# Kernel optimization log

Measured on AMD Instinct MI355X. Metric: run time of the kernel, lower is better.

## Reference

```python
import jax, jax.numpy as jnp
import numpy as np

EPS = 1e-8  # torch F.cosine_similarity default eps
NEG = -1e9  # masked_fill value


def setup_inputs() -> dict:
    key = jax.random.key(0)
    k1, k2, k3 = jax.random.split(key, 3)
    B, Sq, Sk, D = 4, 2048, 2048, 1024
    query = jax.random.normal(k1, (B, Sq, 1, D), dtype=jnp.float32)
    key_t = jax.random.normal(k2, (B, 1, Sk, D), dtype=jnp.float32)
    mask = jax.random.randint(k3, (B, Sk), 0, 2, dtype=jnp.int32)
    return {"query": query, "key": key_t, "mask": mask}


def reference(query, key, mask):
    # query: [B, Sq, 1, D], key: [B, 1, Sk, D]
    q = query[:, :, 0, :]  # [B, Sq, D]
    k = key[:, 0, :, :]    # [B, Sk, D]
    # cosine_similarity(q, k, dim=3) = (q.k) / (max(|q|,eps) * max(|k|,eps))
    qn = jnp.maximum(jnp.linalg.norm(q, axis=-1), EPS)  # [B, Sq]
    kn = jnp.maximum(jnp.linalg.norm(k, axis=-1), EPS)  # [B, Sk]
    dot = jnp.einsum('bqd,bkd->bqk', q, k)              # [B, Sq, Sk]
    scores = dot / (qn[:, :, None] * kn[:, None, :])
    # mask.unsqueeze(1).repeat(1, Sq, 1) -> broadcast [B, 1, Sk] over Sq
    scores = jnp.where(mask[:, None, :] == 0, NEG, scores)
    return scores
```

## Files before the change

### kernel.cpp

```cpp
#include <hip/hip_runtime.h>
#include <hip/hip_bf16.h>
#include <stdint.h>


constexpr int B_  = 4;
constexpr int SQ  = 2048;
constexpr int SK  = 2048;
constexpr int D_  = 1024;
constexpr int BM  = 128;
constexpr int BN  = 128;
constexpr int BK  = 64;

typedef __attribute__((ext_vector_type(8)))  short    short8;
typedef __attribute__((ext_vector_type(4)))  float    f32x4;
typedef __attribute__((ext_vector_type(16))) float    f32x16;
typedef __attribute__((ext_vector_type(4)))  unsigned uint4v;
typedef unsigned int u32;

__device__ inline unsigned pack_bf16(float lo, float hi) {
  union { float f; unsigned u; } a, b;
  a.f = lo; b.f = hi;
  return __builtin_amdgcn_perm(b.u, a.u, 0x07060302u);
}

__device__ inline void async_ld16(const void* g, void* l) {
  __builtin_amdgcn_global_load_lds((const __attribute__((address_space(1))) u32*)g,
                                   (__attribute__((address_space(3))) u32*)l, 16, 0, 0);
}

constexpr int ROWS_Q = B_ * SQ;
constexpr int ROWS_T = B_ * (SQ + SK);

__global__ __launch_bounds__(256) void convert_norm(
    const float* __restrict__ Q, const float* __restrict__ Km,
    unsigned short* __restrict__ Qb, unsigned short* __restrict__ Kb,
    float* __restrict__ invQ, float* __restrict__ invK)
{
  const int row  = blockIdx.x * 4 + (threadIdx.x >> 6);
  const int lane = threadIdx.x & 63;

  const float* src; unsigned short* dst; float* inv;
  if (row < ROWS_Q) {
    src = Q  + (size_t)row * D_;
    dst = Qb + (size_t)row * D_;
    inv = invQ + row;
  } else {
    int r = row - ROWS_Q;
    src = Km + (size_t)r * D_;
    dst = Kb + (size_t)r * D_;
    inv = invK + r;
  }

  const f32x4* s4 = (const f32x4*)(src + lane * 16);
  f32x4 v[4];
  #pragma unroll
  for (int i = 0; i < 4; ++i) v[i] = s4[i];

  float ss = 0.0f;
  unsigned p[8];
  #pragma unroll
  for (int i = 0; i < 4; ++i) {
    p[2*i]   = pack_bf16(v[i].x, v[i].y);
    p[2*i+1] = pack_bf16(v[i].z, v[i].w);
    ss += v[i].x*v[i].x + v[i].y*v[i].y + v[i].z*v[i].z + v[i].w*v[i].w;
  }
  uint4v w0 = {p[0], p[1], p[2], p[3]};
  uint4v w1 = {p[4], p[5], p[6], p[7]};
  uint4v* d4 = (uint4v*)(dst + lane * 16);
  d4[0] = w0; d4[1] = w1;

  #pragma unroll
  for (int off = 32; off > 0; off >>= 1) ss += __shfl_xor(ss, off);
  if (lane == 0) *inv = 1.0f / fmaxf(sqrtf(ss), 1e-8f);
}

__global__ __launch_bounds__(256, 4) void ca_gemm_bf(
    const unsigned short* __restrict__ Qb,
    const unsigned short* __restrict__ Kb,
    const float* __restrict__ invQ,
    const float* __restrict__ invK,
    const int*   __restrict__ mask,
    float*       __restrict__ out)
{
  __shared__ __align__(16) unsigned short As[BM * BK];
  __shared__ __align__(16) unsigned short Bs[BN * BK];

  const int tid  = threadIdx.x;
  const int lane = tid & 63;
  const int w    = tid >> 6;
  const int b    = blockIdx.z;
  const int tm0  = blockIdx.y * BM;
  const int tn0  = blockIdx.x * BN;

  const int srow   = lane >> 3;
  const int gchunk = (lane & 7) ^ srow;

  const char* qrow = (const char*)(Qb + ((size_t)b * SQ + tm0 + w * 32 + srow) * D_) + gchunk * 16;
  const char* krow = (const char*)(Kb + ((size_t)b * SK + tn0 + w * 32 + srow) * D_) + gchunk * 16;
  const size_t rstep8 = (size_t)8 * D_ * 2;

  unsigned short* ldsA = &As[(size_t)(w * 32) * BK];
  unsigned short* ldsB = &Bs[(size_t)(w * 32) * BK];

  f32x16 acc[2][2];
  #pragma unroll
  for (int i = 0; i < 2; ++i)
    #pragma unroll
    for (int j = 0; j < 2; ++j)
      #pragma unroll
      for (int r = 0; r < 16; ++r) acc[i][j][r] = 0.0f;

  const int wm = (w >> 1) * 64;
  const int wn = (w & 1) * 64;
  const int ln = lane & 31;
  const int h  = lane >> 5;

  for (int k0 = 0; k0 < D_; k0 += BK) {
    __syncthreads();
    const size_t kb = (size_t)k0 * 2;
    #pragma unroll
    for (int i = 0; i < 4; ++i)
      async_ld16(qrow + kb + i * rstep8, ldsA + i * 8 * BK);
    #pragma unroll
    for (int i = 0; i < 4; ++i)
      async_ld16(krow + kb + i * rstep8, ldsB + i * 8 * BK);
    __syncthreads();

    #pragma unroll
    for (int s = 0; s < 4; ++s) {
      const int c = 2 * s + h;
      const int ra0 = wm + ln, ra1 = wm + 32 + ln;
      const int rb0 = wn + ln, rb1 = wn + 32 + ln;
      short8 a0 = *(const short8*)&As[(size_t)ra0 * BK + (size_t)((c ^ (ra0 & 7)) * 8)];
      short8 a1 = *(const short8*)&As[(size_t)ra1 * BK + (size_t)((c ^ (ra1 & 7)) * 8)];
      short8 b0 = *(const short8*)&Bs[(size_t)rb0 * BK + (size_t)((c ^ (rb0 & 7)) * 8)];
      short8 b1 = *(const short8*)&Bs[(size_t)rb1 * BK + (size_t)((c ^ (rb1 & 7)) * 8)];
      acc[0][0] = __builtin_amdgcn_mfma_f32_32x32x16_bf16(a0, b0, acc[0][0], 0, 0, 0);
      acc[0][1] = __builtin_amdgcn_mfma_f32_32x32x16_bf16(a0, b1, acc[0][1], 0, 0, 0);
      acc[1][0] = __builtin_amdgcn_mfma_f32_32x32x16_bf16(a1, b0, acc[1][0], 0, 0, 0);
      acc[1][1] = __builtin_amdgcn_mfma_f32_32x32x16_bf16(a1, b1, acc[1][1], 0, 0, 0);
    }
  }

  #pragma unroll
  for (int tj = 0; tj < 2; ++tj) {
    const int gc = tn0 + wn + tj * 32 + ln;
    const int mk = mask[b * SK + gc];
    const float ibv = invK[b * SK + gc];
    #pragma unroll
    for (int ti = 0; ti < 2; ++ti) {
      #pragma unroll
      for (int reg = 0; reg < 16; ++reg) {
        const int row = wm + ti * 32 + (reg & 3) + 8 * (reg >> 2) + 4 * h;
        const float iav = invQ[b * SQ + tm0 + row];
        float v = mk ? acc[ti][tj][reg] * iav * ibv : -1000000000.0f;
        out[((size_t)b * SQ + tm0 + row) * SK + gc] = v;
      }
    }
  }
}

constexpr int LDK = 40;

__global__ __launch_bounds__(256, 2) void ca_gemm(
    const float* __restrict__ Q, const float* __restrict__ Km,
    const int* __restrict__ mask, float* __restrict__ out)
{
  __shared__ __align__(16) short As[BM * LDK];
  __shared__ __align__(16) short Bs[BN * LDK];
  __shared__ float ssA_part[256];
  __shared__ float ssB_part[256];
  __shared__ float invA[BM];
  __shared__ float invB[BN];

  const int tid  = threadIdx.x;
  const int lane = tid & 63;
  const int w    = tid >> 6;
  const int b    = blockIdx.z;
  const int tm0  = blockIdx.y * BM;
  const int tn0  = blockIdx.x * BN;

  const int ra = tid >> 1;
  const int ka = (tid & 1) * 16;

  const float* qp = Q  + ((size_t)b * SQ + tm0 + ra) * D_ + ka;
  const float* kp = Km + ((size_t)b * SK + tn0 + ra) * D_ + ka;

  f32x4 zero4 = {0.0f, 0.0f, 0.0f, 0.0f};
  f32x4 acc[4][4];
  #pragma unroll
  for (int i = 0; i < 4; ++i)
    #pragma unroll
    for (int j = 0; j < 4; ++j) acc[i][j] = zero4;

  float ssA = 0.0f, ssB = 0.0f;

  const int wm = (w >> 1) * 64;
  const int wn = (w & 1) * 64;
  const int lr = lane & 15;
  const int lq = lane >> 4;

  short* aw = &As[ra * LDK + ka];
  short* bw = &Bs[ra * LDK + ka];

  for (int k0 = 0; k0 < D_; k0 += 32) {
    f32x4 av[4], bv[4];
    #pragma unroll
    for (int i = 0; i < 4; ++i) av[i] = *(const f32x4*)(qp + 4 * i);
    #pragma unroll
    for (int i = 0; i < 4; ++i) bv[i] = *(const f32x4*)(kp + 4 * i);
    qp += 32; kp += 32;

    unsigned pa[8], pb[8];
    #pragma unroll
    for (int i = 0; i < 4; ++i) {
      pa[2*i]   = pack_bf16(av[i].x, av[i].y);
      pa[2*i+1] = pack_bf16(av[i].z, av[i].w);
      pb[2*i]   = pack_bf16(bv[i].x, bv[i].y);
      pb[2*i+1] = pack_bf16(bv[i].z, bv[i].w);
      ssA += av[i].x*av[i].x + av[i].y*av[i].y + av[i].z*av[i].z + av[i].w*av[i].w;
      ssB += bv[i].x*bv[i].x + bv[i].y*bv[i].y + bv[i].z*bv[i].z + bv[i].w*bv[i].w;
    }

    __syncthreads();
    {
      uint4v wa0 = {pa[0], pa[1], pa[2], pa[3]};
      uint4v wa1 = {pa[4], pa[5], pa[6], pa[7]};
      uint4v wb0 = {pb[0], pb[1], pb[2], pb[3]};
      uint4v wb1 = {pb[4], pb[5], pb[6], pb[7]};
      *(uint4v*)(aw)     = wa0;
      *(uint4v*)(aw + 8) = wa1;
      *(uint4v*)(bw)     = wb0;
      *(uint4v*)(bw + 8) = wb1;
    }
    __syncthreads();

    short8 af[4], bf[4];
    #pragma unroll
    for (int t = 0; t < 4; ++t)
      af[t] = *(const short8*)&As[(wm + t * 16 + lr) * LDK + lq * 8];
    #pragma unroll
    for (int t = 0; t < 4; ++t)
      bf[t] = *(const short8*)&Bs[(wn + t * 16 + lr) * LDK + lq * 8];

    #pragma unroll
    for (int i = 0; i < 4; ++i)
      #pragma unroll
      for (int j = 0; j < 4; ++j)
        acc[i][j] = __builtin_amdgcn_mfma_f32_16x16x32_bf16(af[i], bf[j], acc[i][j], 0, 0, 0);
  }

  ssA_part[tid] = ssA;
  ssB_part[tid] = ssB;
  __syncthreads();
  if (tid < BM) {
    float s = ssA_part[2 * tid] + ssA_part[2 * tid + 1];
    invA[tid] = 1.0f / fmaxf(sqrtf(s), 1e-8f);
  } else {
    int r = tid - BM;
    float s = ssB_part[2 * r] + ssB_part[2 * r + 1];
    invB[r] = 1.0f / fmaxf(sqrtf(s), 1e-8f);
  }
  __syncthreads();

  #pragma unroll
  for (int tn = 0; tn < 4; ++tn) {
    const int lc = wn + tn * 16 + lr;
    const int gc = tn0 + lc;
    const int mk = mask[b * SK + gc];
    const float ibv = invB[lc];
    #pragma unroll
    for (int tm = 0; tm < 4; ++tm) {
      const int lrow = wm + tm * 16 + lq * 4;
      #pragma unroll
      for (int r = 0; r < 4; ++r) {
        float v = mk ? acc[tm][tn][r] * invA[lrow + r] * ibv : -1000000000.0f;
        out[((size_t)b * SQ + tm0 + lrow + r) * SK + gc] = v;
      }
    }
  }
}

extern "C" void kernel_launch(void* const* d_in, const int* in_sizes, int n_in,
                              void* d_out, int out_size, void* d_ws, size_t ws_size,
                              hipStream_t stream) {
  const float* Q    = (const float*)d_in[0];
  const float* Km   = (const float*)d_in[1];
  const int*   mask = (const int*)d_in[2];
  float*       out  = (float*)d_out;

  const size_t nQ   = (size_t)B_ * SQ * D_;
  const size_t nK   = (size_t)B_ * SK * D_;
  const size_t need = (nQ + nK) * 2 + (size_t)B_ * (SQ + SK) * 4;
  if (ws_size >= need) {
    unsigned short* Qb = (unsigned short*)d_ws;
    unsigned short* Kb = Qb + nQ;
    float*          iQ = (float*)(Kb + nK);
    float*          iK = iQ + (size_t)B_ * SQ;
    convert_norm<<<ROWS_T / 4, 256, 0, stream>>>(Q, Km, Qb, Kb, iQ, iK);
    dim3 grid(SK / BN, SQ / BM, B_);
    ca_gemm_bf<<<grid, dim3(256), 0, stream>>>(Qb, Kb, iQ, iK, mask, out);
  } else {
    dim3 grid(SK / BN, SQ / BM, B_);
    ca_gemm<<<grid, dim3(256), 0, stream>>>(Q, Km, mask, out);
  }
}
```

Measured before the change: 159.3 us.

## Enlarge GEMM tile to 256x256 with triple-buffered async LDS pipeline

The bf16 GEMM kernel moves from 128x128 tiles with BK=64 and 256 threads to 256x256 tiles with BK=32 and 512 threads (8 waves, each computing 128x64). K-slices are staged into three rotating LDS buffers with async global-to-LDS loads and vmcnt-based waits, so loads for future slices overlap MFMA work. Only one barrier per iteration remains instead of two syncthreads. This raises per-block data reuse and hides memory latency, at the cost of a smaller grid (256 blocks), more accumulator registers and a different swizzle.

```diff
diff --git a/kernel.cpp b/kernel.cpp
--- a/kernel.cpp
+++ b/kernel.cpp
@@ -7,9 +7,16 @@
 constexpr int SQ  = 2048;
 constexpr int SK  = 2048;
 constexpr int D_  = 1024;
+
 constexpr int BM  = 128;
 constexpr int BN  = 128;
-constexpr int BK  = 64;
+
+constexpr int BM2 = 256;
+constexpr int BN2 = 256;
+constexpr int BK2 = 32;
+constexpr int NT2 = D_ / BK2;
+constexpr int BUFSH     = BM2 * BK2;
+constexpr int BUFSTRIDE = 2 * BUFSH;
 
 typedef __attribute__((ext_vector_type(8)))  short    short8;
 typedef __attribute__((ext_vector_type(4)))  float    f32x4;
@@ -74,7 +81,7 @@
   if (lane == 0) *inv = 1.0f / fmaxf(sqrtf(ss), 1e-8f);
 }
 
-__global__ __launch_bounds__(256, 4) void ca_gemm_bf(
+__global__ __launch_bounds__(512, 2) void ca_gemm_bf(
     const unsigned short* __restrict__ Qb,
     const unsigned short* __restrict__ Kb,
     const float* __restrict__ invQ,
@@ -82,78 +89,100 @@
     const int*   __restrict__ mask,
     float*       __restrict__ out)
 {
-  __shared__ __align__(16) unsigned short As[BM * BK];
-  __shared__ __align__(16) unsigned short Bs[BN * BK];
+  __shared__ __align__(16) unsigned short lds[3 * BUFSTRIDE];
 
   const int tid  = threadIdx.x;
   const int lane = tid & 63;
   const int w    = tid >> 6;
+  const int wr   = w >> 2;
+  const int wc   = w & 3;
   const int b    = blockIdx.z;
-  const int tm0  = blockIdx.y * BM;
-  const int tn0  = blockIdx.x * BN;
-
-  const int srow   = lane >> 3;
-  const int gchunk = (lane & 7) ^ srow;
-
-  const char* qrow = (const char*)(Qb + ((size_t)b * SQ + tm0 + w * 32 + srow) * D_) + gchunk * 16;
-  const char* krow = (const char*)(Kb + ((size_t)b * SK + tn0 + w * 32 + srow) * D_) + gchunk * 16;
-  const size_t rstep8 = (size_t)8 * D_ * 2;
-
-  unsigned short* ldsA = &As[(size_t)(w * 32) * BK];
-  unsigned short* ldsB = &Bs[(size_t)(w * 32) * BK];
-
-  f32x16 acc[2][2];
-  #pragma unroll
-  for (int i = 0; i < 2; ++i)
-    #pragma unroll
-    for (int j = 0; j < 2; ++j)
+  const int tm0  = blockIdx.y * BM2;
+  const int tn0  = blockIdx.x * BN2;
+
+  const int g = (lane & 3) ^ ((lane >> 3) & 3);
+  const char* qsrc = (const char*)(Qb + ((size_t)b * SQ + tm0 + w * 32 + (lane >> 2)) * D_) + g * 16;
+  const char* ksrc = (const char*)(Kb + ((size_t)b * SK + tn0 + w * 32 + (lane >> 2)) * D_) + g * 16;
+  const size_t RSTEP16 = (size_t)16 * D_ * 2;
+
+  f32x16 acc[4][2];
+  #pragma unroll
+  for (int m = 0; m < 4; ++m)
+    #pragma unroll
+    for (int n = 0; n < 2; ++n)
       #pragma unroll
-      for (int r = 0; r < 16; ++r) acc[i][j][r] = 0.0f;
-
-  const int wm = (w >> 1) * 64;
-  const int wn = (w & 1) * 64;
+      for (int r = 0; r < 16; ++r) acc[m][n][r] = 0.0f;
+
   const int ln = lane & 31;
   const int h  = lane >> 5;
-
-  for (int k0 = 0; k0 < D_; k0 += BK) {
-    __syncthreads();
-    const size_t kb = (size_t)k0 * 2;
-    #pragma unroll
-    for (int i = 0; i < 4; ++i)
-      async_ld16(qrow + kb + i * rstep8, ldsA + i * 8 * BK);
-    #pragma unroll
-    for (int i = 0; i < 4; ++i)
-      async_ld16(krow + kb + i * rstep8, ldsB + i * 8 * BK);
-    __syncthreads();
-
-    #pragma unroll
-    for (int s = 0; s < 4; ++s) {
-      const int c = 2 * s + h;
-      const int ra0 = wm + ln, ra1 = wm + 32 + ln;
-      const int rb0 = wn + ln, rb1 = wn + 32 + ln;
-      short8 a0 = *(const short8*)&As[(size_t)ra0 * BK + (size_t)((c ^ (ra0 & 7)) * 8)];
-      short8 a1 = *(const short8*)&As[(size_t)ra1 * BK + (size_t)((c ^ (ra1 & 7)) * 8)];
-      short8 b0 = *(const short8*)&Bs[(size_t)rb0 * BK + (size_t)((c ^ (rb0 & 7)) * 8)];
-      short8 b1 = *(const short8*)&Bs[(size_t)rb1 * BK + (size_t)((c ^ (rb1 & 7)) * 8)];
+  const int qz = (ln >> 1) & 3;
+
+  auto stage = [&](int bufw) {
+    unsigned short* ba = lds + bufw * BUFSTRIDE + w * 1024;
+    unsigned short* bb = ba + BUFSH;
+    async_ld16(qsrc,           ba);
+    async_ld16(qsrc + RSTEP16, ba + 16 * 32);
+    async_ld16(ksrc,           bb);
+    async_ld16(ksrc + RSTEP16, bb + 16 * 32);
+    qsrc += BK2 * 2;
+    ksrc += BK2 * 2;
+  };
+
+  auto compute = [&](int bufr) {
+    const unsigned short* Ab = lds + bufr * BUFSTRIDE + (wr * 128 + ln) * 32;
+    const unsigned short* Bb = lds + bufr * BUFSTRIDE + BUFSH + (wc * 64 + ln) * 32;
+    #pragma unroll
+    for (int s = 0; s < 2; ++s) {
+      const int p8 = ((2 * s + h) ^ qz) * 8;
+      short8 a0 = *(const short8*)(Ab + p8);
+      short8 a1 = *(const short8*)(Ab + p8 + 1024);
+      short8 a2 = *(const short8*)(Ab + p8 + 2048);
+      short8 a3 = *(const short8*)(Ab + p8 + 3072);
+      short8 b0 = *(const short8*)(Bb + p8);
+      short8 b1 = *(const short8*)(Bb + p8 + 1024);
       acc[0][0] = __builtin_amdgcn_mfma_f32_32x32x16_bf16(a0, b0, acc[0][0], 0, 0, 0);
       acc[0][1] = __builtin_amdgcn_mfma_f32_32x32x16_bf16(a0, b1, acc[0][1], 0, 0, 0);
       acc[1][0] = __builtin_amdgcn_mfma_f32_32x32x16_bf16(a1, b0, acc[1][0], 0, 0, 0);
       acc[1][1] = __builtin_amdgcn_mfma_f32_32x32x16_bf16(a1, b1, acc[1][1], 0, 0, 0);
-    }
-  }
-
-  #pragma unroll
-  for (int tj = 0; tj < 2; ++tj) {
-    const int gc = tn0 + wn + tj * 32 + ln;
+      acc[2][0] = __builtin_amdgcn_mfma_f32_32x32x16_bf16(a2, b0, acc[2][0], 0, 0, 0);
+      acc[2][1] = __builtin_amdgcn_mfma_f32_32x32x16_bf16(a2, b1, acc[2][1], 0, 0, 0);
+      acc[3][0] = __builtin_amdgcn_mfma_f32_32x32x16_bf16(a3, b0, acc[3][0], 0, 0, 0);
+      acc[3][1] = __builtin_amdgcn_mfma_f32_32x32x16_bf16(a3, b1, acc[3][1], 0, 0, 0);
+    }
+  };
+
+  stage(0);
+  stage(1);
+  asm volatile("s_waitcnt vmcnt(4)" ::: "memory");
+  __builtin_amdgcn_s_barrier();
+
+  int bufr = 0, bufw = 2;
+  for (int t = 0; t < NT2; ++t) {
+    if (t < NT2 - 2) {
+      stage(bufw);
+      bufw = (bufw == 2) ? 0 : bufw + 1;
+    }
+    compute(bufr);
+    bufr = (bufr == 2) ? 0 : bufr + 1;
+    if (t < NT2 - 1) {
+      if (t < NT2 - 2) asm volatile("s_waitcnt vmcnt(4)" ::: "memory");
+      else             asm volatile("s_waitcnt vmcnt(0)" ::: "memory");
+      __builtin_amdgcn_s_barrier();
+    }
+  }
+
+  #pragma unroll
+  for (int n = 0; n < 2; ++n) {
+    const int gc = tn0 + wc * 64 + n * 32 + ln;
     const int mk = mask[b * SK + gc];
     const float ibv = invK[b * SK + gc];
     #pragma unroll
-    for (int ti = 0; ti < 2; ++ti) {
+    for (int m = 0; m < 4; ++m) {
       #pragma unroll
       for (int reg = 0; reg < 16; ++reg) {
-        const int row = wm + ti * 32 + (reg & 3) + 8 * (reg >> 2) + 4 * h;
+        const int row = wr * 128 + m * 32 + (reg & 3) + 8 * (reg >> 2) + 4 * h;
         const float iav = invQ[b * SQ + tm0 + row];
-        float v = mk ? acc[ti][tj][reg] * iav * ibv : -1000000000.0f;
+        float v = mk ? acc[m][n][reg] * iav * ibv : -1000000000.0f;
         out[((size_t)b * SQ + tm0 + row) * SK + gc] = v;
       }
     }
@@ -298,8 +327,8 @@
     float*          iQ = (float*)(Kb + nK);
     float*          iK = iQ + (size_t)B_ * SQ;
     convert_norm<<<ROWS_T / 4, 256, 0, stream>>>(Q, Km, Qb, Kb, iQ, iK);
-    dim3 grid(SK / BN, SQ / BM, B_);
-    ca_gemm_bf<<<grid, dim3(256), 0, stream>>>(Qb, Kb, iQ, iK, mask, out);
+    dim3 grid(SK / BN2, SQ / BM2, B_);
+    ca_gemm_bf<<<grid, dim3(512), 0, stream>>>(Qb, Kb, iQ, iK, mask, out);
   } else {
     dim3 grid(SK / BN, SQ / BM, B_);
     ca_gemm<<<grid, dim3(256), 0, stream>>>(Q, Km, mask, out);
```

New measurement: 162.6 us. 1.02x slower.
